# Kernel tuning notes

Hardware: AMD Instinct MI355X
Metric: run time of the kernel (lower is better)

## Reference

```python
import jax, jax.numpy as jnp
import numpy as np

ENC_DIM = 640
DEC_DIM = 640
INNER = 512
VOCAB = 2048


def setup_inputs() -> dict:
    key = jax.random.key(0)
    k1, k2, k3, k4, k5, k6 = jax.random.split(key, 6)
    B, T, U = 4, 256, 64
    enc_state = jax.random.normal(k1, (B, T, ENC_DIM), dtype=jnp.float32)
    dec_state = jax.random.normal(k2, (B, U, DEC_DIM), dtype=jnp.float32)
    s1 = 1.0 / np.sqrt(ENC_DIM + DEC_DIM)
    s2 = 1.0 / np.sqrt(INNER)
    W1 = jax.random.uniform(k3, (INNER, ENC_DIM + DEC_DIM), jnp.float32, -s1, s1)
    b1 = jax.random.uniform(k4, (INNER,), jnp.float32, -s1, s1)
    W2 = jax.random.uniform(k5, (VOCAB, INNER), jnp.float32, -s2, s2)
    b2 = jax.random.uniform(k6, (VOCAB,), jnp.float32, -s2, s2)
    return {"enc_state": enc_state, "dec_state": dec_state,
            "W1": W1, "b1": b1, "W2": W2, "b2": b2}


def reference(enc_state, dec_state, W1, b1, W2, b2):
    # Linear over concat([enc, dec]) == enc @ W_e^T + dec @ W_d^T (split weight),
    # applied over the broadcast T x U grid without materializing the concat tensor.
    We = W1[:, :ENC_DIM]   # [inner, enc_dim]
    Wd = W1[:, ENC_DIM:]   # [inner, dec_dim]
    enc_proj = jnp.einsum('bte,ie->bti', enc_state, We)  # [B,T,inner]
    dec_proj = jnp.einsum('bud,id->bui', dec_state, Wd)  # [B,U,inner]
    h = jnp.tanh(enc_proj[:, :, None, :] + dec_proj[:, None, :, :] + b1)  # [B,T,U,inner]
    logits = jnp.einsum('btui,vi->btuv', h, W2) + b2  # [B,T,U,vocab]
    return logits
```

## Files before the change

### kernel.cpp

```cpp
#include <hip/hip_runtime.h>
#include <hip/hip_bf16.h>
#include <cstdint>
#include <cstddef>


typedef __attribute__((ext_vector_type(8))) short   short8;
typedef __attribute__((ext_vector_type(4))) float   floatx4;

__device__ __forceinline__ short f2bf(float f) {
  union { float f; unsigned u; } v; v.f = f;
  unsigned r = (v.u + 0x7fffu + ((v.u >> 16) & 1u)) >> 16;
  return (short)(unsigned short)r;
}

__device__ __forceinline__ void async16(const void* g, void* l) {
  __builtin_amdgcn_global_load_lds(
      (const __attribute__((address_space(1))) unsigned int*)g,
      (__attribute__((address_space(3))) unsigned int*)l,
      16, 0, 0);
}

__global__ __launch_bounds__(256)
void f32_to_bf16(const float* __restrict__ in, short* __restrict__ out, int n8)
{
  const int i = blockIdx.x * 256 + threadIdx.x;
  if (i >= n8) return;
  const float4* p = (const float4*)in + 2 * (size_t)i;
  const float4 a = p[0], b = p[1];
  short8 o;
  o[0] = f2bf(a.x); o[1] = f2bf(a.y); o[2] = f2bf(a.z); o[3] = f2bf(a.w);
  o[4] = f2bf(b.x); o[5] = f2bf(b.y); o[6] = f2bf(b.z); o[7] = f2bf(b.w);
  ((short8*)out)[i] = o;
}

__global__ __launch_bounds__(256)
void gemm_bt(const short* __restrict__ A, int lda,
             const short* __restrict__ B, int ldb, int bcol,
             float* __restrict__ Cout, int ldc,
             const float* __restrict__ bias, int K)
{
  __shared__ short As[128 * 32];
  __shared__ short Bs[128 * 32];

  const int tid  = threadIdx.x;
  const int lane = tid & 63;
  const int wave = tid >> 6;
  const int wm = (wave >> 1) << 6;
  const int wn = (wave & 1) << 6;
  const int m_base = blockIdx.y * 128;
  const int n_base = blockIdx.x * 128;

  floatx4 acc[4][4];
#pragma unroll
  for (int i = 0; i < 4; i++)
#pragma unroll
    for (int j = 0; j < 4; j++) acc[i][j] = (floatx4)0.0f;

  const short* Ag = A + (size_t)(m_base + (tid >> 2)) * lda + ((tid & 3) * 8);
  const short* Bg = B + (size_t)(n_base + (tid >> 2)) * ldb + bcol + ((tid & 3) * 8);
  short* Al = &As[tid * 8];
  short* Bl = &Bs[tid * 8];
  const size_t aHalf = (size_t)64 * lda;
  const size_t bHalf = (size_t)64 * ldb;

  const int ak   = (lane >> 4) * 8;
  const int arow = lane & 15;

  for (int kb = 0; kb < K; kb += 32) {
    __syncthreads();
    async16(Ag + kb,         Al);
    async16(Ag + kb + aHalf, Al + 2048);
    async16(Bg + kb,         Bl);
    async16(Bg + kb + bHalf, Bl + 2048);
    __syncthreads();

    short8 af[4], bfr[4];
#pragma unroll
    for (int i = 0; i < 4; i++)
      af[i] = *(const short8*)&As[(wm + i * 16 + arow) * 32 + ak];
#pragma unroll
    for (int j = 0; j < 4; j++)
      bfr[j] = *(const short8*)&Bs[(wn + j * 16 + arow) * 32 + ak];
#pragma unroll
    for (int i = 0; i < 4; i++)
#pragma unroll
      for (int j = 0; j < 4; j++)
        acc[i][j] = __builtin_amdgcn_mfma_f32_16x16x32_bf16(af[i], bfr[j], acc[i][j], 0, 0, 0);
  }

  const int quad = lane >> 4;
  const int coll = lane & 15;
  float bv[4] = {0.f, 0.f, 0.f, 0.f};
  if (bias) {
#pragma unroll
    for (int j = 0; j < 4; j++) bv[j] = bias[n_base + wn + j * 16 + coll];
  }
#pragma unroll
  for (int i = 0; i < 4; i++) {
#pragma unroll
    for (int r = 0; r < 4; r++) {
      const size_t row = (size_t)(m_base + wm + i * 16 + quad * 4 + r);
#pragma unroll
      for (int j = 0; j < 4; j++) {
        const size_t off = row * (size_t)ldc + (n_base + wn + j * 16 + coll);
        Cout[off] = acc[i][j][r] + bv[j];
      }
    }
  }
}

__global__ __launch_bounds__(256)
void tanh_fuse(const float* __restrict__ Pe, const float* __restrict__ Pd,
               const float* __restrict__ b1, short* __restrict__ H, int m0)
{
  const int idx = blockIdx.x * 256 + threadIdx.x;
  const int lm = idx >> 6;
  const int c = (idx & 63) << 3;
  const int m = m0 + lm;
  const int b = m >> 14;
  const int t = (m >> 6) & 255;
  const int u = m & 63;

  const float* pe = Pe + (size_t)((b << 8) + t) * 512 + c;
  const float* pd = Pd + (size_t)((b << 6) + u) * 512 + c;
  const float4 e0 = *(const float4*)pe;
  const float4 e1 = *(const float4*)(pe + 4);
  const float4 d0 = *(const float4*)pd;
  const float4 d1 = *(const float4*)(pd + 4);
  const float4 g0 = *(const float4*)(b1 + c);
  const float4 g1 = *(const float4*)(b1 + c + 4);

  float x[8] = {e0.x + d0.x + g0.x, e0.y + d0.y + g0.y,
                e0.z + d0.z + g0.z, e0.w + d0.w + g0.w,
                e1.x + d1.x + g1.x, e1.y + d1.y + g1.y,
                e1.z + d1.z + g1.z, e1.w + d1.w + g1.w};
  short8 o;
#pragma unroll
  for (int j = 0; j < 8; j++) {
    const float e  = __expf(2.0f * x[j]);
    const float th = 1.0f - 2.0f / (e + 1.0f);
    o[j] = f2bf(th);
  }
  *(short8*)(H + (size_t)lm * 512 + c) = o;
}

extern "C" void kernel_launch(void* const* d_in, const int* in_sizes, int n_in,
                              void* d_out, int out_size, void* d_ws, size_t ws_size,
                              hipStream_t stream)
{
  const float* enc = (const float*)d_in[0];
  const float* dec = (const float*)d_in[1];
  const float* W1  = (const float*)d_in[2];
  const float* b1  = (const float*)d_in[3];
  const float* W2  = (const float*)d_in[4];
  const float* b2  = (const float*)d_in[5];
  float* out = (float*)d_out;

  size_t off = 0;
  auto carve = [&](size_t bytes) -> void* {
    void* p = (char*)d_ws + off;
    off += (bytes + 255) & ~(size_t)255;
    return p;
  };
  short* encb = (short*)carve(1024 * 640 * 2);
  short* decb = (short*)carve(256 * 640 * 2);
  short* W1b  = (short*)carve(512 * 1280 * 2);
  short* W2b  = (short*)carve(2048 * 512 * 2);
  float* Pe   = (float*)carve(1024 * 512 * 4);
  float* Pd   = (float*)carve(256 * 512 * 4);
  short* H    = (short*)((char*)d_ws + off);

  const size_t avail = (ws_size > off) ? (ws_size - off) : 0;
  long long rpc = (long long)(avail / (512 * 2));
  rpc = (rpc / 128) * 128;
  if (rpc < 128) rpc = 128;
  if (rpc > 65536) rpc = 65536;

  auto cgrid = [](int n8) { return (unsigned)((n8 + 255) / 256); };
  const int n8_enc = 1024 * 640 / 8;
  const int n8_dec = 256 * 640 / 8;
  const int n8_W1  = 512 * 1280 / 8;
  const int n8_W2  = 2048 * 512 / 8;
  f32_to_bf16<<<cgrid(n8_enc), 256, 0, stream>>>(enc, encb, n8_enc);
  f32_to_bf16<<<cgrid(n8_dec), 256, 0, stream>>>(dec, decb, n8_dec);
  f32_to_bf16<<<cgrid(n8_W1),  256, 0, stream>>>(W1,  W1b,  n8_W1);
  f32_to_bf16<<<cgrid(n8_W2),  256, 0, stream>>>(W2,  W2b,  n8_W2);

  gemm_bt<<<dim3(4, 8), 256, 0, stream>>>(encb, 640, W1b, 1280, 0,   Pe, 512, nullptr, 640);
  gemm_bt<<<dim3(4, 2), 256, 0, stream>>>(decb, 640, W1b, 1280, 640, Pd, 512, nullptr, 640);

  for (long long m0 = 0; m0 < 65536; m0 += rpc) {
    const long long rows = (65536 - m0 < rpc) ? (65536 - m0) : rpc;
    tanh_fuse<<<(unsigned)(rows / 4), 256, 0, stream>>>(Pe, Pd, b1, H, (int)m0);
    gemm_bt<<<dim3(16, (unsigned)(rows / 128)), 256, 0, stream>>>(
        H, 512, W2b, 512, 0, out + (size_t)m0 * 2048, 2048, b2, 512);
  }
}
```

Before: 730.0 us.

## Replace bf16 GEMM with triple-buffered 128x256 tile pipeline and XCD-aware block mapping

Replaces the single-buffered 128x128 GEMM, which synchronised twice per K step, with a 512-thread kernel. The new kernel uses 128x256 tiles, K chunks of 64, and three dynamic LDS buffers filled by async global-to-LDS loads two tiles ahead. It adds an XOR swizzle on LDS layout to avoid bank conflicts, a workgroup remap across the 8 XCDs, and split staging interleaved with MFMA bursts under raised wave priority. The aim is to hide global load latency and keep the matrix units busy. In exchange it needs about 144KB of LDS per block, which limits occupancy to one block per CU, and it adds a one-time attribute set.

New measurement: 714.2 us. -2.2%, faster.

```diff
diff --git a/kernel.cpp b/kernel.cpp
--- a/kernel.cpp
+++ b/kernel.cpp
@@ -33,22 +33,44 @@
   ((short8*)out)[i] = o;
 }
 
-__global__ __launch_bounds__(256)
-void gemm_bt(const short* __restrict__ A, int lda,
-             const short* __restrict__ B, int ldb, int bcol,
-             float* __restrict__ Cout, int ldc,
-             const float* __restrict__ bias, int K)
-{
-  __shared__ short As[128 * 32];
-  __shared__ short Bs[128 * 32];
-
+#define BUFB 49152
+
+__global__ __launch_bounds__(512, 2)
+void gemm_pipe(const short* __restrict__ A, int lda,
+               const short* __restrict__ B, int ldb, int bcol,
+               float* __restrict__ Cout, int ldc,
+               const float* __restrict__ bias, int K, int nbx_sh)
+{
+  extern __shared__ char lds[];
   const int tid  = threadIdx.x;
   const int lane = tid & 63;
-  const int wave = tid >> 6;
-  const int wm = (wave >> 1) << 6;
-  const int wn = (wave & 1) << 6;
-  const int m_base = blockIdx.y * 128;
-  const int n_base = blockIdx.x * 128;
+  const int w    = tid >> 6;
+  const int wm   = (w >> 2) << 6;
+  const int wn   = (w & 3) << 6;
+
+  const int nwg = gridDim.x;
+  const int qq = nwg >> 3, rr = nwg & 7;
+  const int xcd = blockIdx.x & 7, idx = blockIdx.x >> 3;
+  const int wg = (xcd < rr ? xcd * (qq + 1) : rr * (qq + 1) + (xcd - rr) * qq) + idx;
+  const int nbx_mask = (1 << nbx_sh) - 1;
+  const int m_base = (wg >> nbx_sh) << 7;
+  const int n_base = (wg & nbx_mask) << 8;
+
+  const int srow = tid >> 3;
+  const int sblk = (tid & 7) ^ (srow & 7);
+  const short* Asrc = A + (size_t)(m_base + srow) * lda + (sblk << 3);
+  const short* Bsrc = B + (size_t)(n_base + srow) * ldb + bcol + (sblk << 3);
+  const size_t a64 = (size_t)64 * lda;
+  const size_t b64 = (size_t)64 * ldb;
+  char* const ldst = lds + tid * 16;
+
+  const int arow = lane & 15;
+  const int q4   = lane >> 4;
+  const int s7   = arow & 7;
+  const int koff0 = ((q4)     ^ s7) << 4;
+  const int koff1 = ((q4 + 4) ^ s7) << 4;
+  const size_t aoff = (size_t)(wm + arow) * 128;
+  const size_t boff = 16384 + (size_t)(wn + arow) * 128;
 
   floatx4 acc[4][4];
 #pragma unroll
@@ -56,36 +78,77 @@
 #pragma unroll
     for (int j = 0; j < 4; j++) acc[i][j] = (floatx4)0.0f;
 
-  const short* Ag = A + (size_t)(m_base + (tid >> 2)) * lda + ((tid & 3) * 8);
-  const short* Bg = B + (size_t)(n_base + (tid >> 2)) * ldb + bcol + ((tid & 3) * 8);
-  short* Al = &As[tid * 8];
-  short* Bl = &Bs[tid * 8];
-  const size_t aHalf = (size_t)64 * lda;
-  const size_t bHalf = (size_t)64 * ldb;
-
-  const int ak   = (lane >> 4) * 8;
-  const int arow = lane & 15;
-
-  for (int kb = 0; kb < K; kb += 32) {
-    __syncthreads();
-    async16(Ag + kb,         Al);
-    async16(Ag + kb + aHalf, Al + 2048);
-    async16(Bg + kb,         Bl);
-    async16(Bg + kb + bHalf, Bl + 2048);
-    __syncthreads();
-
-    short8 af[4], bfr[4];
+  const int NT = K >> 6;
+
+#pragma unroll
+  for (int t = 0; t < 2; ++t) {
+    const int kb = t << 6;
+    char* dA = ldst + t * BUFB;
+    char* dB = dA + 16384;
+    async16(Asrc + kb,             dA);
+    async16(Asrc + kb + a64,       dA + 8192);
+    async16(Bsrc + kb,             dB);
+    async16(Bsrc + kb + b64,       dB + 8192);
+    async16(Bsrc + kb + 2 * b64,   dB + 16384);
+    async16(Bsrc + kb + 3 * b64,   dB + 24576);
+  }
+
+  int r = 0;
+  for (int kt = 0; kt < NT; ++kt) {
+    if (kt + 1 < NT) asm volatile("s_waitcnt vmcnt(6)" ::: "memory");
+    else             asm volatile("s_waitcnt vmcnt(0)" ::: "memory");
+    __builtin_amdgcn_s_barrier();
+    asm volatile("" ::: "memory");
+
+    const char* Ab = lds + r * BUFB + aoff;
+    const char* Bb = lds + r * BUFB + boff;
+    const int r2 = (r >= 1) ? r - 1 : 2;
+    char* dA = ldst + r2 * BUFB;
+    char* dB = dA + 16384;
+    const int  kb2 = (kt + 2) << 6;
+    const bool do_stage = (kt + 2 < NT);
+
+    short8 af[4], bf[4];
+
+#pragma unroll
+    for (int i = 0; i < 4; i++) af[i] = *(const short8*)(Ab + i * 2048 + koff0);
+#pragma unroll
+    for (int j = 0; j < 4; j++) bf[j] = *(const short8*)(Bb + j * 2048 + koff0);
+    if (do_stage) {
+      async16(Asrc + kb2,           dA);
+      async16(Asrc + kb2 + a64,     dA + 8192);
+      async16(Bsrc + kb2,           dB);
+    }
+    __builtin_amdgcn_s_barrier();
+    asm volatile("s_waitcnt lgkmcnt(0)" ::: "memory");
+    __builtin_amdgcn_s_setprio(1);
 #pragma unroll
     for (int i = 0; i < 4; i++)
-      af[i] = *(const short8*)&As[(wm + i * 16 + arow) * 32 + ak];
-#pragma unroll
-    for (int j = 0; j < 4; j++)
-      bfr[j] = *(const short8*)&Bs[(wn + j * 16 + arow) * 32 + ak];
+#pragma unroll
+      for (int j = 0; j < 4; j++)
+        acc[i][j] = __builtin_amdgcn_mfma_f32_16x16x32_bf16(af[i], bf[j], acc[i][j], 0, 0, 0);
+    __builtin_amdgcn_s_setprio(0);
+
+#pragma unroll
+    for (int i = 0; i < 4; i++) af[i] = *(const short8*)(Ab + i * 2048 + koff1);
+#pragma unroll
+    for (int j = 0; j < 4; j++) bf[j] = *(const short8*)(Bb + j * 2048 + koff1);
+    if (do_stage) {
+      async16(Bsrc + kb2 + b64,     dB + 8192);
+      async16(Bsrc + kb2 + 2 * b64, dB + 16384);
+      async16(Bsrc + kb2 + 3 * b64, dB + 24576);
+    }
+    __builtin_amdgcn_s_barrier();
+    asm volatile("s_waitcnt lgkmcnt(0)" ::: "memory");
+    __builtin_amdgcn_s_setprio(1);
 #pragma unroll
     for (int i = 0; i < 4; i++)
 #pragma unroll
       for (int j = 0; j < 4; j++)
-        acc[i][j] = __builtin_amdgcn_mfma_f32_16x16x32_bf16(af[i], bfr[j], acc[i][j], 0, 0, 0);
+        acc[i][j] = __builtin_amdgcn_mfma_f32_16x16x32_bf16(af[i], bf[j], acc[i][j], 0, 0, 0);
+    __builtin_amdgcn_s_setprio(0);
+
+    r = (r == 2) ? 0 : r + 1;
   }
 
   const int quad = lane >> 4;
@@ -98,12 +161,12 @@
 #pragma unroll
   for (int i = 0; i < 4; i++) {
 #pragma unroll
-    for (int r = 0; r < 4; r++) {
-      const size_t row = (size_t)(m_base + wm + i * 16 + quad * 4 + r);
+    for (int rr2 = 0; rr2 < 4; rr2++) {
+      const size_t row = (size_t)(m_base + wm + i * 16 + quad * 4 + rr2);
 #pragma unroll
       for (int j = 0; j < 4; j++) {
         const size_t off = row * (size_t)ldc + (n_base + wn + j * 16 + coll);
-        Cout[off] = acc[i][j][r] + bv[j];
+        Cout[off] = acc[i][j][rr2] + bv[j];
       }
     }
   }
@@ -155,6 +218,13 @@
   const float* W2  = (const float*)d_in[4];
   const float* b2  = (const float*)d_in[5];
   float* out = (float*)d_out;
+
+  static bool attr_done = false;
+  if (!attr_done) {
+    hipFuncSetAttribute((const void*)gemm_pipe,
+                        hipFuncAttributeMaxDynamicSharedMemorySize, 3 * BUFB);
+    attr_done = true;
+  }
 
   size_t off = 0;
   auto carve = [&](size_t bytes) -> void* {
@@ -186,13 +256,15 @@
   f32_to_bf16<<<cgrid(n8_W1),  256, 0, stream>>>(W1,  W1b,  n8_W1);
   f32_to_bf16<<<cgrid(n8_W2),  256, 0, stream>>>(W2,  W2b,  n8_W2);
 
-  gemm_bt<<<dim3(4, 8), 256, 0, stream>>>(encb, 640, W1b, 1280, 0,   Pe, 512, nullptr, 640);
-  gemm_bt<<<dim3(4, 2), 256, 0, stream>>>(decb, 640, W1b, 1280, 640, Pd, 512, nullptr, 640);
+  gemm_pipe<<<16, 512, 3 * BUFB, stream>>>(encb, 640, W1b, 1280, 0,
+                                           Pe, 512, nullptr, 640, 1);
+  gemm_pipe<<<4, 512, 3 * BUFB, stream>>>(decb, 640, W1b, 1280, 640,
+                                          Pd, 512, nullptr, 640, 1);
 
   for (long long m0 = 0; m0 < 65536; m0 += rpc) {
     const long long rows = (65536 - m0 < rpc) ? (65536 - m0) : rpc;
     tanh_fuse<<<(unsigned)(rows / 4), 256, 0, stream>>>(Pe, Pd, b1, H, (int)m0);
-    gemm_bt<<<dim3(16, (unsigned)(rows / 128)), 256, 0, stream>>>(
-        H, 512, W2b, 512, 0, out + (size_t)m0 * 2048, 2048, b2, 512);
-  }
-}
+    gemm_pipe<<<(unsigned)(8 * (rows / 128)), 512, 3 * BUFB, stream>>>(
+        H, 512, W2b, 512, 0, out + (size_t)m0 * 2048, 2048, b2, 512, 3);
+  }
+}
```
